# Kernel tuning notes

Hardware: AMD Instinct MI355X
Metric: run time of the kernel (lower is better)

## Reference

```python
import jax, jax.numpy as jnp
import numpy as np

K = 2          # neighbors per point (init default k=2)
ALPHA = 5e-4   # regularization weight (init default)
N_CLASSES = 1000


def setup_inputs() -> dict:
    key = jax.random.key(0)
    k1, k2, k3 = jax.random.split(key, 3)
    n, d_feat, n_cls = 4096, 1024, N_CLASSES
    x_batch = jax.random.normal(k1, (n, d_feat), dtype=jnp.float32)
    y_batch = jax.random.randint(k2, (n,), 0, n_cls, dtype=jnp.int32)
    y_output = jax.random.normal(k3, (n, n_cls), dtype=jnp.float32)
    return {"x_batch": x_batch, "y_batch": y_batch, "y_output": y_output}


def _pairwise_dist(a):
    # ||a_i - a_j|| via gram trick; clamp for numerical safety.
    sq = jnp.sum(a * a, axis=-1)                       # [n]
    d2 = sq[:, None] + sq[None, :] - 2.0 * (a @ a.T)   # [n, n]
    d2 = jnp.maximum(d2, 0.0)
    # sqrt with zero-safe gradient (diag / coincident points)
    safe = jnp.where(d2 > 0.0, d2, 1.0)
    return jnp.where(d2 > 0.0, jnp.sqrt(safe), 0.0)


def reference(x_batch, y_batch, y_output):
    n = x_batch.shape[0]
    d = _pairwise_dist(x_batch)                        # [n, n] input-space distances

    # K nearest neighbors, excluding self (i != j in the original loops)
    d_knn = d + jnp.where(jnp.eye(n, dtype=bool), jnp.inf, 0.0)
    _, nbr_idx = jax.lax.top_k(-d_knn, K)              # [n, K] smallest distances
    nbr_mask = jnp.zeros((n, n), dtype=d.dtype)
    nbr_mask = nbr_mask.at[jnp.arange(n)[:, None], nbr_idx].set(1.0)

    same_class = (y_batch[:, None] == y_batch[None, :])
    w = jnp.exp(-d) * nbr_mask                         # exp(-d) on KNN edges only
    # w_diff = w_int - w_pen: +exp(-d) for same-class neighbors, -exp(-d) otherwise
    w_diff = jnp.where(same_class, w, -w)

    y_norm = _pairwise_dist(y_output)                  # [n, n] ||y_out_i - y_out_j||
    reg_value = jnp.sum(w_diff * y_norm)
    return ALPHA * reg_value
```

## Files before the change

### kernel.cpp

```cpp
#include <hip/hip_runtime.h>
#include <math.h>

#define ALPHA 5e-4f
#define BIG 1e30f

typedef __attribute__((ext_vector_type(4))) float f32x4;

__device__ __forceinline__ void gload16(const void* g, void* l) {
    __builtin_amdgcn_global_load_lds(
        (const __attribute__((address_space(1))) void*)g,
        (__attribute__((address_space(3))) void*)l, 16, 0, 0);
}

__global__ __launch_bounds__(256)
void conv_fp8_kernel(const float* __restrict__ X, unsigned char* __restrict__ Xq,
                     float* __restrict__ sqn32, int d) {
    const int w = threadIdx.x >> 6, lane = threadIdx.x & 63;
    const int row = blockIdx.x * 4 + w;
    const float4* src = reinterpret_cast<const float4*>(X + (size_t)row * d);
    int4* dst = reinterpret_cast<int4*>(Xq + (size_t)row * d);
    float s = 0.f;
    const int ng = d >> 4;
    for (int g = lane; g < ng; g += 64) {
        int wds[4];
#pragma unroll
        for (int q = 0; q < 4; ++q) {
            float4 v = src[g * 4 + q];
            s += v.x * v.x + v.y * v.y + v.z * v.z + v.w * v.w;
            int t0 = __builtin_amdgcn_cvt_pk_fp8_f32(v.x, v.y, 0, false);
            wds[q] = __builtin_amdgcn_cvt_pk_fp8_f32(v.z, v.w, t0, true);
        }
        dst[g] = make_int4(wds[0], wds[1], wds[2], wds[3]);
    }
    for (int off = 1; off < 64; off <<= 1) s += __shfl_xor(s, off, 64);
    if (lane == 0) sqn32[row] = s;
}

#define BM 128
#define BN 128
#define BKB 64

__global__ __launch_bounds__(256, 4)
void gram_top2_mfma(const unsigned char* __restrict__ Xq, const float* __restrict__ sqn,
                    float* __restrict__ cand_s, int* __restrict__ cand_i,
                    int n, int d, int nbc, int cpx) {
    __shared__ unsigned char As[2][BM * BKB];
    __shared__ unsigned char Bs[2][BN * BKB];

    const int bid = blockIdx.x;
    const int swz = (bid & 7) * cpx + (bid >> 3);
    const int rb = swz >> 5, cb = swz & 31;

    const int row0 = rb * BM, col0 = cb * BN;
    const int t = threadIdx.x;
    const int w = t >> 6, l = t & 63;
    const int wr = w >> 1, wc = w & 1;
    const int lc = l & 15, lg = l >> 4;

    f32x4 acc[4][4];
#pragma unroll
    for (int i = 0; i < 4; ++i)
#pragma unroll
        for (int j = 0; j < 4; ++j) acc[i][j] = (f32x4){0.f, 0.f, 0.f, 0.f};

    const int gsw = ((t & 3) ^ ((t >> 3) & 3)) << 4;
    const size_t gA0 = (size_t)(row0 + (t >> 2)) * d + gsw;
    const size_t gB0 = (size_t)(col0 + (t >> 2)) * d + gsw;
    const size_t rstep = (size_t)64 * d;
    const int wbase = w * 1024;
    const int rsw = ((lc >> 1) & 3) << 1;

    const int nsteps = d / BKB;

#define STAGE(stg, ks)                                            \
    {                                                             \
        const size_t ko = (size_t)(ks) * BKB;                     \
        gload16(Xq + gA0 + ko, As[stg] + wbase);                  \
        gload16(Xq + gA0 + ko + rstep, As[stg] + wbase + 4096);   \
        gload16(Xq + gB0 + ko, Bs[stg] + wbase);                  \
        gload16(Xq + gB0 + ko + rstep, Bs[stg] + wbase + 4096);   \
    }

    STAGE(0, 0)
    int cur = 0;
    for (int ks = 0; ks < nsteps; ++ks) {
        if (ks + 1 < nsteps) {
            STAGE(cur ^ 1, ks + 1)
            asm volatile("s_waitcnt vmcnt(4)" ::: "memory");
        } else {
            asm volatile("s_waitcnt vmcnt(0)" ::: "memory");
        }
        __builtin_amdgcn_s_barrier();

        long long a[2][4], b[2][4];
#pragma unroll
        for (int ki = 0; ki < 2; ++ki) {
            const int ch = ((ki * 4 + lg) ^ rsw) * 8;
#pragma unroll
            for (int mi = 0; mi < 4; ++mi) {
                a[ki][mi] = *reinterpret_cast<const long long*>(
                    &As[cur][(wr * 64 + mi * 16 + lc) * 64 + ch]);
                b[ki][mi] = *reinterpret_cast<const long long*>(
                    &Bs[cur][(wc * 64 + mi * 16 + lc) * 64 + ch]);
            }
        }
        __builtin_amdgcn_s_setprio(1);
#pragma unroll
        for (int mi = 0; mi < 4; ++mi)
#pragma unroll
            for (int ni = 0; ni < 4; ++ni) {
                acc[mi][ni] = __builtin_amdgcn_mfma_f32_16x16x32_fp8_fp8(
                    a[0][mi], b[0][ni], acc[mi][ni], 0, 0, 0);
                acc[mi][ni] = __builtin_amdgcn_mfma_f32_16x16x32_fp8_fp8(
                    a[1][mi], b[1][ni], acc[mi][ni], 0, 0, 0);
            }
        __builtin_amdgcn_s_setprio(0);

        asm volatile("s_waitcnt lgkmcnt(0)" ::: "memory");
        __builtin_amdgcn_s_barrier();
        cur ^= 1;
    }
#undef STAGE

    float sq_c[4];
#pragma unroll
    for (int ni = 0; ni < 4; ++ni) sq_c[ni] = sqn[col0 + wc * 64 + ni * 16 + lc];
    const int strip_r = cb * 2 + wc;

#pragma unroll
    for (int mi = 0; mi < 4; ++mi) {
#pragma unroll
        for (int j = 0; j < 4; ++j) {
            const int grow = row0 + wr * 64 + mi * 16 + lg * 4 + j;
            float s1v = BIG, s2v = BIG;
            int i1 = -1, i2 = -1;
#pragma unroll
            for (int ni = 0; ni < 4; ++ni) {
                const int gcol = col0 + wc * 64 + ni * 16 + lc;
                float s = sq_c[ni] - 2.f * acc[mi][ni][j];
                if (gcol == grow) s = BIG;
                if (s < s1v) { s2v = s1v; i2 = i1; s1v = s; i1 = gcol; }
                else if (s < s2v) { s2v = s; i2 = gcol; }
            }
            for (int off = 1; off < 16; off <<= 1) {
                float b1 = __shfl_xor(s1v, off, 16);
                int  bi1 = __shfl_xor(i1, off, 16);
                float b2 = __shfl_xor(s2v, off, 16);
                int  bi2 = __shfl_xor(i2, off, 16);
                if (b1 < s1v) { s2v = s1v; i2 = i1; s1v = b1; i1 = bi1; }
                else if (b1 < s2v) { s2v = b1; i2 = bi1; }
                if (b2 < s2v) { s2v = b2; i2 = bi2; }
            }
            if (lc == 0) {
                size_t base = ((size_t)grow * 64 + strip_r) * 2;
                cand_s[base] = s1v; cand_s[base + 1] = s2v;
                cand_i[base] = i1; cand_i[base + 1] = i2;
            }
        }
    }
}

__global__ __launch_bounds__(256)
void merge_edges_kernel(const float* __restrict__ sqn,
                        const float* __restrict__ cand_s, const int* __restrict__ cand_i,
                        const int* __restrict__ yb, const float* __restrict__ yo,
                        float* __restrict__ partial, int ncls) {
    const int w = threadIdx.x >> 6, lane = threadIdx.x & 63;
    const int row = blockIdx.x * 4 + w;

    float2 cs = reinterpret_cast<const float2*>(cand_s + (size_t)row * 128)[lane];
    int2   ci = reinterpret_cast<const int2*>(cand_i + (size_t)row * 128)[lane];
    float s1 = cs.x, s2 = cs.y;
    int i1 = ci.x, i2 = ci.y;
    if (s2 < s1) { float ts = s1; s1 = s2; s2 = ts; int ti = i1; i1 = i2; i2 = ti; }

    for (int off = 1; off < 64; off <<= 1) {
        float b1 = __shfl_xor(s1, off, 64);
        int  bi1 = __shfl_xor(i1, off, 64);
        float b2 = __shfl_xor(s2, off, 64);
        int  bi2 = __shfl_xor(i2, off, 64);
        if (b1 < s1) { s2 = s1; i2 = i1; s1 = b1; i1 = bi1; }
        else if (b1 < s2) { s2 = b1; i2 = bi1; }
        if (b2 < s2) { s2 = b2; i2 = bi2; }
    }
    const int yr = yb[row];
    const float sr = sqn[row];
    float w1 = ((yr == yb[i1]) ? 1.f : -1.f) * expf(-sqrtf(fmaxf(sr + s1, 0.f)));
    float w2 = ((yr == yb[i2]) ? 1.f : -1.f) * expf(-sqrtf(fmaxf(sr + s2, 0.f)));

    const float4* yr4 = reinterpret_cast<const float4*>(yo + (size_t)row * ncls);
    const float4* y14 = reinterpret_cast<const float4*>(yo + (size_t)i1 * ncls);
    const float4* y24 = reinterpret_cast<const float4*>(yo + (size_t)i2 * ncls);
    const int nv4 = ncls >> 2;
    float a1 = 0.f, a2 = 0.f;
    for (int c = lane; c < nv4; c += 64) {
        float4 v = yr4[c];
        float4 u1 = y14[c];
        float4 u2 = y24[c];
        float tx = v.x - u1.x, ty = v.y - u1.y, tz = v.z - u1.z, tw = v.w - u1.w;
        a1 = fmaf(tx, tx, fmaf(ty, ty, fmaf(tz, tz, fmaf(tw, tw, a1))));
        tx = v.x - u2.x; ty = v.y - u2.y; tz = v.z - u2.z; tw = v.w - u2.w;
        a2 = fmaf(tx, tx, fmaf(ty, ty, fmaf(tz, tz, fmaf(tw, tw, a2))));
    }
    for (int c = (nv4 << 2) + lane; c < ncls; c += 64) {
        float v = yo[(size_t)row * ncls + c];
        float t1 = v - yo[(size_t)i1 * ncls + c];
        float t2 = v - yo[(size_t)i2 * ncls + c];
        a1 = fmaf(t1, t1, a1);
        a2 = fmaf(t2, t2, a2);
    }
    for (int off = 1; off < 64; off <<= 1) {
        a1 += __shfl_xor(a1, off, 64);
        a2 += __shfl_xor(a2, off, 64);
    }
    if (lane == 0)
        partial[row] = w1 * sqrtf(a1) + w2 * sqrtf(a2);
}

__global__ __launch_bounds__(256)
void final_reduce_kernel(const float* __restrict__ partial, float* __restrict__ out, int n) {
    const int t = threadIdx.x;
    __shared__ float red[4];
    float s = 0.f;
    const int nv4 = n >> 2;
    const float4* p4 = reinterpret_cast<const float4*>(partial);
    for (int c = t; c < nv4; c += 256) {
        float4 v = p4[c];
        s += v.x + v.y + v.z + v.w;
    }
    for (int off = 1; off < 64; off <<= 1) s += __shfl_xor(s, off, 64);
    if ((t & 63) == 0) red[t >> 6] = s;
    __syncthreads();
    if (t == 0) out[0] = ALPHA * (red[0] + red[1] + red[2] + red[3]);
}

extern "C" void kernel_launch(void* const* d_in, const int* in_sizes, int n_in,
                              void* d_out, int out_size, void* d_ws, size_t ws_size,
                              hipStream_t stream) {
    const float* X  = (const float*)d_in[0];
    const int*   yb = (const int*)d_in[1];
    const float* yo = (const float*)d_in[2];
    float* out = (float*)d_out;

    const int n    = in_sizes[1];
    const int d    = in_sizes[0] / n;
    const int ncls = in_sizes[2] / n;
    const int nbc  = n / BM;

    char* wsb = (char*)d_ws;
    size_t off = 0;
    float* sqn32 = (float*)(wsb + off);         off += ((size_t)n * 4 + 255) & ~(size_t)255;
    unsigned char* Xq = (unsigned char*)(wsb + off); off += ((size_t)n * d + 255) & ~(size_t)255;
    float* cand_s = (float*)(wsb + off);        off += ((size_t)n * 64 * 2 * 4 + 255) & ~(size_t)255;
    int*   cand_i = (int*)(wsb + off);          off += ((size_t)n * 64 * 2 * 4 + 255) & ~(size_t)255;
    float* partial = (float*)(wsb + off);

    conv_fp8_kernel<<<n / 4, 256, 0, stream>>>(X, Xq, sqn32, d);

    const int nsq = nbc * nbc;
    const int cpx = nsq / 8;
    gram_top2_mfma<<<nsq, 256, 0, stream>>>(Xq, sqn32, cand_s, cand_i, n, d, nbc, cpx);

    merge_edges_kernel<<<n / 4, 256, 0, stream>>>(sqn32, cand_s, cand_i, yb, yo, partial, ncls);

    final_reduce_kernel<<<1, 256, 0, stream>>>(partial, out, n);
}
```

Before: 58.77 us.

## Enlarge gram tiles to 256x256 with 512 threads and 4-stage pipeline

The FP8 gram/top-2 kernel goes from 128x128 tiles with 256 threads and double buffering to 256x256 tiles with 8 waves, each computing 128x64, and a 4-deep LDS ring with staggered A/B prefetch. The larger tiles raise arithmetic intensity and cut global traffic per MFMA, and the deeper pipeline hides load latency. In exchange it uses 128KB of LDS and many more accumulator registers, which lowers occupancy, and the grid shrinks to 256 blocks, fewer waves of work for the GPU's CUs. The candidate strip layout stays at 64 strips per row via cb*4+wcn.

```diff
diff --git a/kernel.cpp b/kernel.cpp
--- a/kernel.cpp
+++ b/kernel.cpp
@@ -36,107 +36,125 @@
     if (lane == 0) sqn32[row] = s;
 }
 
-#define BM 128
-#define BN 128
-#define BKB 64
-
-__global__ __launch_bounds__(256, 4)
+#define BMQ 256
+#define TKB 64
+
+__global__ __launch_bounds__(512)
 void gram_top2_mfma(const unsigned char* __restrict__ Xq, const float* __restrict__ sqn,
                     float* __restrict__ cand_s, int* __restrict__ cand_i,
                     int n, int d, int nbc, int cpx) {
-    __shared__ unsigned char As[2][BM * BKB];
-    __shared__ unsigned char Bs[2][BN * BKB];
+    __shared__ unsigned char As[4][BMQ * TKB];
+    __shared__ unsigned char Bs[4][BMQ * TKB];
 
     const int bid = blockIdx.x;
     const int swz = (bid & 7) * cpx + (bid >> 3);
-    const int rb = swz >> 5, cb = swz & 31;
-
-    const int row0 = rb * BM, col0 = cb * BN;
+    const int rb = swz >> 4, cb = swz & 15;
+
+    const int row0 = rb * BMQ, col0 = cb * BMQ;
     const int t = threadIdx.x;
     const int w = t >> 6, l = t & 63;
-    const int wr = w >> 1, wc = w & 1;
+    const int wr = w >> 2, wcn = w & 3;
     const int lc = l & 15, lg = l >> 4;
 
-    f32x4 acc[4][4];
-#pragma unroll
-    for (int i = 0; i < 4; ++i)
+    f32x4 acc[8][4];
+#pragma unroll
+    for (int i = 0; i < 8; ++i)
 #pragma unroll
         for (int j = 0; j < 4; ++j) acc[i][j] = (f32x4){0.f, 0.f, 0.f, 0.f};
 
-    const int gsw = ((t & 3) ^ ((t >> 3) & 3)) << 4;
-    const size_t gA0 = (size_t)(row0 + (t >> 2)) * d + gsw;
-    const size_t gB0 = (size_t)(col0 + (t >> 2)) * d + gsw;
-    const size_t rstep = (size_t)64 * d;
-    const int wbase = w * 1024;
-    const int rsw = ((lc >> 1) & 3) << 1;
-
-    const int nsteps = d / BKB;
-
-#define STAGE(stg, ks)                                            \
-    {                                                             \
-        const size_t ko = (size_t)(ks) * BKB;                     \
-        gload16(Xq + gA0 + ko, As[stg] + wbase);                  \
-        gload16(Xq + gA0 + ko + rstep, As[stg] + wbase + 4096);   \
-        gload16(Xq + gB0 + ko, Bs[stg] + wbase);                  \
-        gload16(Xq + gB0 + ko + rstep, Bs[stg] + wbase + 4096);   \
-    }
-
-    STAGE(0, 0)
-    int cur = 0;
-    for (int ks = 0; ks < nsteps; ++ks) {
-        if (ks + 1 < nsteps) {
-            STAGE(cur ^ 1, ks + 1)
-            asm volatile("s_waitcnt vmcnt(4)" ::: "memory");
-        } else {
-            asm volatile("s_waitcnt vmcnt(0)" ::: "memory");
+    const int srow = w * 16 + (l >> 2);
+    const int sblk = ((l & 3) ^ ((l >> 3) & 3)) << 4;
+    const size_t gA0 = (size_t)(row0 + srow) * d + sblk;
+    const size_t gB0 = (size_t)(col0 + srow) * d + sblk;
+    const size_t hstep = (size_t)128 * d;
+    const int wb = w * 1024;
+
+    const int nt = d / TKB;
+
+#define STAGE_A(bi, ks)                                                   \
+    {                                                                     \
+        const size_t ko = (size_t)(ks) * TKB;                             \
+        gload16(Xq + gA0 + ko, As[bi] + wb);                              \
+        gload16(Xq + gA0 + ko + hstep, As[bi] + wb + 8192);               \
+    }
+#define STAGE_B(bi, ks)                                                   \
+    {                                                                     \
+        const size_t ko = (size_t)(ks) * TKB;                             \
+        gload16(Xq + gB0 + ko, Bs[bi] + wb);                              \
+        gload16(Xq + gB0 + ko + hstep, Bs[bi] + wb + 8192);               \
+    }
+
+    STAGE_A(0, 0) STAGE_B(0, 0)
+    STAGE_A(1, 1) STAGE_B(1, 1)
+    STAGE_A(2, 2) STAGE_B(2, 2)
+    asm volatile("s_waitcnt vmcnt(8)" ::: "memory");
+    __builtin_amdgcn_s_barrier();
+
+    const int csw = ((lc >> 1) & 3) << 1;
+
+    for (int ks = 0; ks < nt; ++ks) {
+        const int bi = ks & 3;
+        const int sb = (ks + 3) & 3;
+        const bool st = (ks + 3) < nt;
+
+#pragma unroll
+        for (int ww = 0; ww < 2; ++ww) {
+            long long a[8], b[4];
+            const int ch = ((ww * 4 + lg) ^ csw) * 8;
+#pragma unroll
+            for (int mi = 0; mi < 8; ++mi)
+                a[mi] = *reinterpret_cast<const long long*>(
+                    &As[bi][(wr * 128 + mi * 16 + lc) * TKB + ch]);
+#pragma unroll
+            for (int ni = 0; ni < 4; ++ni)
+                b[ni] = *reinterpret_cast<const long long*>(
+                    &Bs[bi][(wcn * 64 + ni * 16 + lc) * TKB + ch]);
+
+            if (st) {
+                if (ww == 0) { STAGE_A(sb, ks + 3) }
+                else         { STAGE_B(sb, ks + 3) }
+            }
+            __builtin_amdgcn_s_barrier();
+
+            __builtin_amdgcn_s_setprio(1);
+#pragma unroll
+            for (int mi = 0; mi < 8; ++mi)
+#pragma unroll
+                for (int ni = 0; ni < 4; ++ni)
+                    acc[mi][ni] = __builtin_amdgcn_mfma_f32_16x16x32_fp8_fp8(
+                        a[mi], b[ni], acc[mi][ni], 0, 0, 0);
+            __builtin_amdgcn_s_setprio(0);
+
+            if (ww == 1) {
+                if (ks <= nt - 4) {
+                    asm volatile("s_waitcnt vmcnt(8)" ::: "memory");
+                } else if (ks == nt - 3) {
+                    asm volatile("s_waitcnt vmcnt(4)" ::: "memory");
+                } else if (ks == nt - 2) {
+                    asm volatile("s_waitcnt vmcnt(0)" ::: "memory");
+                }
+            }
+            __builtin_amdgcn_s_barrier();
         }
-        __builtin_amdgcn_s_barrier();
-
-        long long a[2][4], b[2][4];
-#pragma unroll
-        for (int ki = 0; ki < 2; ++ki) {
-            const int ch = ((ki * 4 + lg) ^ rsw) * 8;
-#pragma unroll
-            for (int mi = 0; mi < 4; ++mi) {
-                a[ki][mi] = *reinterpret_cast<const long long*>(
-                    &As[cur][(wr * 64 + mi * 16 + lc) * 64 + ch]);
-                b[ki][mi] = *reinterpret_cast<const long long*>(
-                    &Bs[cur][(wc * 64 + mi * 16 + lc) * 64 + ch]);
-            }
-        }
-        __builtin_amdgcn_s_setprio(1);
-#pragma unroll
-        for (int mi = 0; mi < 4; ++mi)
-#pragma unroll
-            for (int ni = 0; ni < 4; ++ni) {
-                acc[mi][ni] = __builtin_amdgcn_mfma_f32_16x16x32_fp8_fp8(
-                    a[0][mi], b[0][ni], acc[mi][ni], 0, 0, 0);
-                acc[mi][ni] = __builtin_amdgcn_mfma_f32_16x16x32_fp8_fp8(
-                    a[1][mi], b[1][ni], acc[mi][ni], 0, 0, 0);
-            }
-        __builtin_amdgcn_s_setprio(0);
-
-        asm volatile("s_waitcnt lgkmcnt(0)" ::: "memory");
-        __builtin_amdgcn_s_barrier();
-        cur ^= 1;
-    }
-#undef STAGE
+    }
+#undef STAGE_A
+#undef STAGE_B
 
     float sq_c[4];
 #pragma unroll
-    for (int ni = 0; ni < 4; ++ni) sq_c[ni] = sqn[col0 + wc * 64 + ni * 16 + lc];
-    const int strip_r = cb * 2 + wc;
-
-#pragma unroll
-    for (int mi = 0; mi < 4; ++mi) {
+    for (int ni = 0; ni < 4; ++ni) sq_c[ni] = sqn[col0 + wcn * 64 + ni * 16 + lc];
+    const int strip_r = cb * 4 + wcn;
+
+#pragma unroll
+    for (int mi = 0; mi < 8; ++mi) {
 #pragma unroll
         for (int j = 0; j < 4; ++j) {
-            const int grow = row0 + wr * 64 + mi * 16 + lg * 4 + j;
+            const int grow = row0 + wr * 128 + mi * 16 + lg * 4 + j;
             float s1v = BIG, s2v = BIG;
             int i1 = -1, i2 = -1;
 #pragma unroll
             for (int ni = 0; ni < 4; ++ni) {
-                const int gcol = col0 + wc * 64 + ni * 16 + lc;
+                const int gcol = col0 + wcn * 64 + ni * 16 + lc;
                 float s = sq_c[ni] - 2.f * acc[mi][ni][j];
                 if (gcol == grow) s = BIG;
                 if (s < s1v) { s2v = s1v; i2 = i1; s1v = s; i1 = gcol; }
@@ -245,7 +263,7 @@
     const int n    = in_sizes[1];
     const int d    = in_sizes[0] / n;
     const int ncls = in_sizes[2] / n;
-    const int nbc  = n / BM;
+    const int nbc  = n / BMQ;
 
     char* wsb = (char*)d_ws;
     size_t off = 0;
@@ -259,7 +277,7 @@
 
     const int nsq = nbc * nbc;
     const int cpx = nsq / 8;
-    gram_top2_mfma<<<nsq, 256, 0, stream>>>(Xq, sqn32, cand_s, cand_i, n, d, nbc, cpx);
+    gram_top2_mfma<<<nsq, 512, 0, stream>>>(Xq, sqn32, cand_s, cand_i, n, d, nbc, cpx);
 
     merge_edges_kernel<<<n / 4, 256, 0, stream>>>(sqn32, cand_s, cand_i, yb, yo, partial, ncls);
 
```

New measurement: 66.73 us. +13.6%, slower.
